# Kernel tuning notes

Hardware: AMD Instinct MI355X
Metric: run time of the kernel (lower is better)

The kernel has to match this reference:

```python
import jax, jax.numpy as jnp
import numpy as np

N_NODES = 100000
N_EDGES = 1600000
IN_FEATS, HID, NUM_CLS = 128, 128, 40


def setup_inputs() -> dict:
    key = jax.random.key(0)
    ks = jax.random.split(key, 5)
    x = jax.random.normal(ks[0], (N_NODES, IN_FEATS), dtype=jnp.float32)
    # xavier-like scale for weights
    W1 = jax.random.normal(ks[1], (IN_FEATS, HID), dtype=jnp.float32) * (1.0 / np.sqrt(IN_FEATS))
    b1 = jnp.zeros((HID,), dtype=jnp.float32)
    W2 = jax.random.normal(ks[2], (HID, NUM_CLS), dtype=jnp.float32) * (1.0 / np.sqrt(HID))
    b2 = jnp.zeros((NUM_CLS,), dtype=jnp.float32)
    src = jax.random.randint(ks[3], (N_EDGES,), 0, N_NODES, dtype=jnp.int32)
    dst = jax.random.randint(ks[4], (N_EDGES,), 0, N_NODES, dtype=jnp.int32)
    return {"x": x, "W1": W1, "b1": b1, "W2": W2, "b2": b2, "src": src, "dst": dst}


def _graph_conv(h, W, b, src, dst, src_norm, dst_norm, n_nodes):
    # DGL GraphConv, norm='both': D_out^{-1/2} A D_in^{-1/2} H W + b
    # (weight-first vs aggregate-first ordering in DGL is mathematically identical)
    hs = h * src_norm[:, None]                      # [N, d] source-side norm
    msg = hs[src]                                   # [E, d] gather
    agg = jax.ops.segment_sum(msg, dst, num_segments=n_nodes)  # [N, d] scatter-add
    agg = agg * dst_norm[:, None]                   # dest-side norm
    return agg @ W + b


def reference(x, W1, b1, W2, b2, src, dst):
    n = x.shape[0]
    ones = jnp.ones(src.shape[0], dtype=x.dtype)
    out_deg = jnp.clip(jax.ops.segment_sum(ones, src, num_segments=n), 1.0)
    in_deg = jnp.clip(jax.ops.segment_sum(ones, dst, num_segments=n), 1.0)
    src_norm = out_deg ** -0.5
    dst_norm = in_deg ** -0.5
    h = jax.nn.relu(_graph_conv(x, W1, b1, src, dst, src_norm, dst_norm, n))
    return _graph_conv(h, W2, b2, src, dst, src_norm, dst_norm, n)
```

## Files before the change

kernel.cpp:

```cpp
#include <hip/hip_runtime.h>

constexpr int NN   = 100000;
constexpr int NE   = 1600000;
constexpr int INF  = 128;
constexpr int NC   = 40;
constexpr int HPAD = 64;

constexpr int BKSH = 9;
constexpr int NBK  = (NN + 511) / 512;
constexpr int CAPB = 10240;
constexpr int EPB  = 4096;
constexpr int PBLK = (NE + EPB - 1) / EPB;
constexpr int CVB  = 6250;
constexpr int ATS  = 136;

typedef __attribute__((ext_vector_type(8))) short short8;
typedef __attribute__((ext_vector_type(4))) float f32x4;

__device__ __forceinline__ float bflo(unsigned int u) { return __uint_as_float(u << 16); }
__device__ __forceinline__ float bfhi(unsigned int u) { return __uint_as_float(u & 0xffff0000u); }
__device__ __forceinline__ unsigned short f2bf(float f) {
    unsigned int u = __float_as_uint(f);
    return (unsigned short)((u + 0x7fffu + ((u >> 16) & 1u)) >> 16);
}
__device__ __forceinline__ unsigned int pack2(float a, float b) {
    return (unsigned int)f2bf(a) | ((unsigned int)f2bf(b) << 16);
}

__global__ __launch_bounds__(256) void partconv_kernel(const int* __restrict__ src,
                                                       const int* __restrict__ dst,
                                                       int* __restrict__ curD_g,
                                                       int* __restrict__ curS_g,
                                                       int* __restrict__ epartsD,
                                                       unsigned short* __restrict__ epartsS,
                                                       const float* __restrict__ x,
                                                       unsigned short* __restrict__ xh,
                                                       const float* __restrict__ W1,
                                                       const float* __restrict__ W2,
                                                       unsigned short* __restrict__ w1t,
                                                       unsigned short* __restrict__ w2t) {
    const int tid = threadIdx.x;
    if (blockIdx.x >= PBLK) {
        int cb = blockIdx.x - PBLK;
        if (cb < CVB) {
            int j = cb * 256 + tid;
            float4 v0 = ((const float4*)x)[2 * j];
            float4 v1 = ((const float4*)x)[2 * j + 1];
            uint4 o;
            o.x = pack2(v0.x, v0.y);
            o.y = pack2(v0.z, v0.w);
            o.z = pack2(v1.x, v1.y);
            o.w = pack2(v1.z, v1.w);
            ((uint4*)xh)[j] = o;
        } else if (cb == CVB) {
            for (int i = tid; i < 128 * 128; i += 256) {
                int k = i >> 7, n = i & 127;
                w1t[n * 128 + k] = f2bf(W1[i]);
            }
        } else {
            for (int i = tid; i < 48 * 128; i += 256) {
                int n = i >> 7, k = i & 127;
                w2t[i] = f2bf((n < NC) ? W2[k * NC + n] : 0.f);
            }
        }
        return;
    }
    __shared__ int sc[256];
    __shared__ int cntD[NBK], gadjD[NBK], curD[NBK];
    __shared__ int cntS[NBK], gadjS[NBK], curS[NBK];
    __shared__ int stageD[EPB];
    __shared__ unsigned short stageS[EPB];
    __shared__ unsigned char bidD[EPB];
    __shared__ unsigned char bidS[EPB];
    const int e0 = blockIdx.x * EPB;
    const int total = min(EPB, NE - e0);

    for (int i = tid; i < NBK; i += 256) { cntD[i] = 0; cntS[i] = 0; }
    __syncthreads();
    for (int i = tid; i < total; i += 256) {
        atomicAdd(&cntD[dst[e0 + i] >> BKSH], 1);
        atomicAdd(&cntS[src[e0 + i] >> BKSH], 1);
    }
    __syncthreads();
    {
        int v = (tid < NBK) ? cntD[tid] : 0;
        sc[tid] = v;
        __syncthreads();
        for (int off = 1; off < 256; off <<= 1) {
            int t = (tid >= off) ? sc[tid - off] : 0;
            __syncthreads();
            sc[tid] += t;
            __syncthreads();
        }
        if (tid < NBK) {
            int excl = sc[tid] - v;
            curD[tid] = excl;
            int g = (v > 0) ? atomicAdd(&curD_g[tid], v) : 0;
            gadjD[tid] = tid * CAPB + g - excl;
        }
        __syncthreads();
        v = (tid < NBK) ? cntS[tid] : 0;
        sc[tid] = v;
        __syncthreads();
        for (int off = 1; off < 256; off <<= 1) {
            int t = (tid >= off) ? sc[tid - off] : 0;
            __syncthreads();
            sc[tid] += t;
            __syncthreads();
        }
        if (tid < NBK) {
            int excl = sc[tid] - v;
            curS[tid] = excl;
            int g = (v > 0) ? atomicAdd(&curS_g[tid], v) : 0;
            gadjS[tid] = tid * CAPB + g - excl;
        }
    }
    __syncthreads();
    for (int i = tid; i < total; i += 256) {
        int s = src[e0 + i];
        int d = dst[e0 + i];
        int bD = d >> BKSH;
        int offD = atomicAdd(&curD[bD], 1);
        stageD[offD] = s | ((d - (bD << BKSH)) << 17);
        bidD[offD] = (unsigned char)bD;
        int bS = s >> BKSH;
        int offS = atomicAdd(&curS[bS], 1);
        stageS[offS] = (unsigned short)(s - (bS << BKSH));
        bidS[offS] = (unsigned char)bS;
    }
    __syncthreads();
    for (int j = tid; j < total; j += 256) {
        int b = bidD[j];
        epartsD[gadjD[b] + j] = stageD[j];
    }
    for (int j = tid; j < total; j += 256) {
        int b = bidS[j];
        epartsS[gadjS[b] + j] = stageS[j];
    }
}

__global__ __launch_bounds__(1024) void pass2_kernel(const int* __restrict__ epartsD,
                                                     const unsigned short* __restrict__ epartsS,
                                                     const int* __restrict__ curD_g,
                                                     const int* __restrict__ curS_g,
                                                     int* __restrict__ row_beg,
                                                     int* __restrict__ row_end,
                                                     int* __restrict__ esrc,
                                                     float* __restrict__ srcn,
                                                     float* __restrict__ dstn) {
    __shared__ int hist[512];
    __shared__ int cur[512];
    __shared__ int histS[512];
    __shared__ int lesrc[CAPB];
    const int tid = threadIdx.x;
    const int b = blockIdx.x;

    const int base  = b * CAPB;
    const int cnt   = curD_g[b];
    const int cntS  = curS_g[b];
    const int n0 = b << BKSH;
    const int nloc = min(512, NN - n0);

    if (tid < 512) { hist[tid] = 0; histS[tid] = 0; }
    __syncthreads();
    for (int j = tid; j < cnt; j += 1024)
        atomicAdd(&hist[epartsD[base + j] >> 17], 1);
    for (int j = tid; j < cntS; j += 1024)
        atomicAdd(&histS[(int)epartsS[base + j]], 1);
    __syncthreads();
    int myc  = (tid < 512) ? hist[tid] : 0;
    int mycS = (tid < 512) ? histS[tid] : 0;
    for (int off = 1; off < 512; off <<= 1) {
        int t = (tid < 512 && tid >= off) ? hist[tid - off] : 0;
        __syncthreads();
        if (tid < 512) hist[tid] += t;
        __syncthreads();
    }
    if (tid < 512) {
        int excl = hist[tid] - myc;
        cur[tid] = excl;
        if (tid < nloc) {
            int g = n0 + tid;
            row_beg[g] = base + excl;
            row_end[g] = base + excl + myc;
            dstn[g] = rsqrtf(fmaxf((float)myc, 1.0f));
            srcn[g] = rsqrtf(fmaxf((float)mycS, 1.0f));
        }
    }
    __syncthreads();
    for (int j = tid; j < cnt; j += 1024) {
        int rec = epartsD[base + j];
        int pos = atomicAdd(&cur[rec >> 17], 1);
        lesrc[pos] = rec & 0x1FFFF;
    }
    __syncthreads();
    for (int j = tid; j < cnt; j += 1024) esrc[base + j] = lesrc[j];
}

__global__ __launch_bounds__(256, 8) void fused_kernel(const int* __restrict__ row_beg,
                                                       const int* __restrict__ row_end,
                                                       const int* __restrict__ esrc,
                                                       const unsigned short* __restrict__ xh,
                                                       const float* __restrict__ srcn,
                                                       const unsigned short* __restrict__ w1t,
                                                       const unsigned short* __restrict__ w2t,
                                                       const float* __restrict__ b1,
                                                       const float* __restrict__ dstn,
                                                       unsigned short* __restrict__ hwb) {
    __shared__ unsigned short At[32 * ATS];
    __shared__ float dn[32], sn[32], b1l[128];
    const int tid  = threadIdx.x;
    const int r0   = blockIdx.x * 32;
    const int wv   = tid >> 6;
    const int lane = tid & 63;

    if (tid < 32) {
        int r = r0 + tid;
        dn[tid] = (r < NN) ? dstn[r] : 0.f;
        sn[tid] = (r < NN) ? srcn[r] : 0.f;
    }
    if (tid >= 64 && tid < 192) b1l[tid - 64] = b1[tid - 64];
    __syncthreads();

    const int quad = lane >> 4;
    const int l16  = lane & 15;
    for (int i = 0; i < 8; ++i) {
        const int node = r0 + wv * 8 + i;
        float a0 = 0.f, a1 = 0.f, a2 = 0.f, a3 = 0.f;
        float a4 = 0.f, a5 = 0.f, a6 = 0.f, a7 = 0.f;
        if (node < NN) {
            int beg = __builtin_amdgcn_readfirstlane(row_beg[node]);
            int end = __builtin_amdgcn_readfirstlane(row_end[node]);
            for (int e = beg; e < end; e += 16) {
                const int rem = end - e;
                int s[4];
#pragma unroll
                for (int t = 0; t < 4; ++t) {
                    int slot = t * 4 + quad;
                    s[t] = esrc[(slot < rem) ? (e + slot) : beg];
                }
                float n[4];
                uint4 u[4];
#pragma unroll
                for (int t = 0; t < 4; ++t) {
                    int slot = t * 4 + quad;
                    n[t] = (slot < rem) ? srcn[s[t]] : 0.f;
                    u[t] = ((const uint4*)(xh + (size_t)s[t] * INF))[l16];
                }
#pragma unroll
                for (int t = 0; t < 4; ++t) {
                    a0 += bflo(u[t].x) * n[t]; a1 += bfhi(u[t].x) * n[t];
                    a2 += bflo(u[t].y) * n[t]; a3 += bfhi(u[t].y) * n[t];
                    a4 += bflo(u[t].z) * n[t]; a5 += bfhi(u[t].z) * n[t];
                    a6 += bflo(u[t].w) * n[t]; a7 += bfhi(u[t].w) * n[t];
                }
            }
        }
        a0 += __shfl_down(a0, 32); a1 += __shfl_down(a1, 32);
        a2 += __shfl_down(a2, 32); a3 += __shfl_down(a3, 32);
        a4 += __shfl_down(a4, 32); a5 += __shfl_down(a5, 32);
        a6 += __shfl_down(a6, 32); a7 += __shfl_down(a7, 32);
        a0 += __shfl_down(a0, 16); a1 += __shfl_down(a1, 16);
        a2 += __shfl_down(a2, 16); a3 += __shfl_down(a3, 16);
        a4 += __shfl_down(a4, 16); a5 += __shfl_down(a5, 16);
        a6 += __shfl_down(a6, 16); a7 += __shfl_down(a7, 16);
        if (lane < 16) {
            uint4 o;
            o.x = pack2(a0, a1);
            o.y = pack2(a2, a3);
            o.z = pack2(a4, a5);
            o.w = pack2(a6, a7);
            *(uint4*)&At[(wv * 8 + i) * ATS + l16 * 8] = o;
        }
    }
    __syncthreads();

    const int lrow  = lane & 15;
    const int lquad = lane >> 4;
    const int rt    = wv >> 1;
    const int ntB   = (wv & 1) * 4;

    short8 afrag[4];
#pragma unroll
    for (int ks = 0; ks < 4; ++ks)
        afrag[ks] = *(const short8*)&At[(rt * 16 + lrow) * ATS + ks * 32 + lquad * 8];
    __syncthreads();

    float hreg[4][4];
#pragma unroll
    for (int nt2 = 0; nt2 < 4; ++nt2) {
        f32x4 acc = {0.f, 0.f, 0.f, 0.f};
#pragma unroll
        for (int ks = 0; ks < 4; ++ks) {
            short8 bfr = *(const short8*)&w1t[((ntB + nt2) * 16 + lrow) * 128 + ks * 32 + lquad * 8];
            acc = __builtin_amdgcn_mfma_f32_16x16x32_bf16(afrag[ks], bfr, acc, 0, 0, 0);
        }
#pragma unroll
        for (int i = 0; i < 4; ++i) hreg[nt2][i] = acc[i];
    }
#pragma unroll
    for (int nt2 = 0; nt2 < 4; ++nt2) {
        int col = (ntB + nt2) * 16 + lrow;
        float bb = b1l[col];
#pragma unroll
        for (int i = 0; i < 4; ++i) {
            int row = rt * 16 + lquad * 4 + i;
            At[row * ATS + col] = f2bf(fmaxf(hreg[nt2][i] * dn[row] + bb, 0.f));
        }
    }
    __syncthreads();

    if ((wv & 1) == 0) {
        short8 hf[4];
#pragma unroll
        for (int ks = 0; ks < 4; ++ks)
            hf[ks] = *(const short8*)&At[(rt * 16 + lrow) * ATS + ks * 32 + lquad * 8];
#pragma unroll
        for (int nt = 0; nt < 3; ++nt) {
            f32x4 acc = {0.f, 0.f, 0.f, 0.f};
#pragma unroll
            for (int ks = 0; ks < 4; ++ks) {
                short8 bfr = *(const short8*)&w2t[(nt * 16 + lrow) * 128 + ks * 32 + lquad * 8];
                acc = __builtin_amdgcn_mfma_f32_16x16x32_bf16(hf[ks], bfr, acc, 0, 0, 0);
            }
            int col = nt * 16 + lrow;
            if (col < NC) {
#pragma unroll
                for (int i = 0; i < 4; ++i) {
                    int row = rt * 16 + lquad * 4 + i;
                    int grow = r0 + row;
                    if (grow < NN)
                        hwb[(size_t)grow * HPAD + col] = f2bf(acc[i] * sn[row]);
                }
            }
        }
    }
}

__global__ __launch_bounds__(256) void gather2_kernel(const int* __restrict__ row_beg,
                                                      const int* __restrict__ row_end,
                                                      const int* __restrict__ esrc,
                                                      const unsigned short* __restrict__ hwb,
                                                      const float* __restrict__ dst_norm,
                                                      const float* __restrict__ b2,
                                                      float* __restrict__ out) {
    int node = (blockIdx.x * blockDim.x + threadIdx.x) >> 6;
    int lane = threadIdx.x & 63;
    if (node >= NN) return;
    int beg = __builtin_amdgcn_readfirstlane(row_beg[node]);
    int end = __builtin_amdgcn_readfirstlane(row_end[node]);
    const int g = lane >> 3;
    const int j = lane & 7;
    float a0 = 0.f, a1 = 0.f, a2 = 0.f, a3 = 0.f;
    float a4 = 0.f, a5 = 0.f, a6 = 0.f, a7 = 0.f;
    for (int e = beg; e < end; e += 32) {
        const int rem = end - e;
        int s[4];
        float m[4];
#pragma unroll
        for (int q = 0; q < 4; ++q) {
            int slot = q * 8 + g;
            bool v = (slot < rem);
            s[q] = esrc[v ? (e + slot) : beg];
            m[q] = v ? 1.f : 0.f;
        }
        uint4 u[4];
#pragma unroll
        for (int q = 0; q < 4; ++q)
            u[q] = ((const uint4*)(hwb + (size_t)s[q] * HPAD))[j];
#pragma unroll
        for (int q = 0; q < 4; ++q) {
            a0 += bflo(u[q].x) * m[q]; a1 += bfhi(u[q].x) * m[q];
            a2 += bflo(u[q].y) * m[q]; a3 += bfhi(u[q].y) * m[q];
            a4 += bflo(u[q].z) * m[q]; a5 += bfhi(u[q].z) * m[q];
            a6 += bflo(u[q].w) * m[q]; a7 += bfhi(u[q].w) * m[q];
        }
    }
    a0 += __shfl_down(a0, 32); a1 += __shfl_down(a1, 32);
    a2 += __shfl_down(a2, 32); a3 += __shfl_down(a3, 32);
    a4 += __shfl_down(a4, 32); a5 += __shfl_down(a5, 32);
    a6 += __shfl_down(a6, 32); a7 += __shfl_down(a7, 32);
    a0 += __shfl_down(a0, 16); a1 += __shfl_down(a1, 16);
    a2 += __shfl_down(a2, 16); a3 += __shfl_down(a3, 16);
    a4 += __shfl_down(a4, 16); a5 += __shfl_down(a5, 16);
    a6 += __shfl_down(a6, 16); a7 += __shfl_down(a7, 16);
    a0 += __shfl_down(a0, 8);  a1 += __shfl_down(a1, 8);
    a2 += __shfl_down(a2, 8);  a3 += __shfl_down(a3, 8);
    a4 += __shfl_down(a4, 8);  a5 += __shfl_down(a5, 8);
    a6 += __shfl_down(a6, 8);  a7 += __shfl_down(a7, 8);
    if (lane < 5) {
        float dnv = dst_norm[node];
        float4 bb0 = ((const float4*)b2)[2 * lane];
        float4 bb1 = ((const float4*)b2)[2 * lane + 1];
        float4 o0, o1;
        o0.x = a0 * dnv + bb0.x;
        o0.y = a1 * dnv + bb0.y;
        o0.z = a2 * dnv + bb0.z;
        o0.w = a3 * dnv + bb0.w;
        o1.x = a4 * dnv + bb1.x;
        o1.y = a5 * dnv + bb1.y;
        o1.z = a6 * dnv + bb1.z;
        o1.w = a7 * dnv + bb1.w;
        float4* op = (float4*)(out + (size_t)node * NC);
        op[2 * lane]     = o0;
        op[2 * lane + 1] = o1;
    }
}

extern "C" void kernel_launch(void* const* d_in, const int* in_sizes, int n_in,
                              void* d_out, int out_size, void* d_ws, size_t ws_size,
                              hipStream_t stream) {
    const float* x   = (const float*)d_in[0];
    const float* W1  = (const float*)d_in[1];
    const float* b1  = (const float*)d_in[2];
    const float* W2  = (const float*)d_in[3];
    const float* b2  = (const float*)d_in[4];
    const int*   src = (const int*)d_in[5];
    const int*   dst = (const int*)d_in[6];
    float* out = (float*)d_out;

    float* srcn = (float*)d_ws;
    int* curDg = (int*)(srcn + NN);
    int* curSg = curDg + 256;
    int* row_beg = curSg + 256;
    int* row_end = row_beg + NN;
    float* dstn  = (float*)(row_end + NN);
    int* esrc    = (int*)(dstn + NN);
    size_t ofs = (size_t)NN + 512 + 3 * (size_t)NN + (size_t)NBK * CAPB;
    ofs = (ofs + 3) & ~(size_t)3;
    unsigned short* xh   = (unsigned short*)((float*)d_ws + ofs);
    unsigned short* w1t  = xh + (size_t)NN * INF;
    unsigned short* w2t  = w1t + 128 * 128;
    unsigned short* hwb  = w2t + 48 * 128;

    int* epartsD = (int*)d_out;
    unsigned short* epartsS = (unsigned short*)(epartsD + (size_t)NBK * CAPB);

    hipMemsetAsync(curDg, 0, 512 * sizeof(int), stream);

    partconv_kernel<<<PBLK + CVB + 2, 256, 0, stream>>>(src, dst, curDg, curSg,
                                                        epartsD, epartsS,
                                                        x, xh, W1, W2, w1t, w2t);
    pass2_kernel<<<NBK, 1024, 0, stream>>>(epartsD, epartsS, curDg, curSg,
                                           row_beg, row_end, esrc, srcn, dstn);
    fused_kernel<<<(NN + 31) / 32, 256, 0, stream>>>(row_beg, row_end, esrc, xh,
                                                     srcn, w1t, w2t, b1, dstn, hwb);
    gather2_kernel<<<(NN * 64 + 255) / 256, 256, 0, stream>>>(row_beg, row_end,
                                                              esrc, hwb,
                                                              dstn, b2, out);
}
```

Before: 272.8 us.

## Move x/weight bf16 conversion into pass2 and speed up partition scan

The x/W1/W2 bf16 conversion blocks move from the partition kernel into the pass2 kernel, so the conversion now overlaps the per-bucket CSR build instead of the edge partitioning. The partition kernel keeps src/dst in registers between the count and scatter passes, which avoids a second global read. It also replaces the two barrier-heavy shared-memory scans with a wavefront shuffle scan that handles both histograms at once. The cost is higher register pressure (32 ints per thread) and 1024-thread conversion blocks sharing the launch with the heavy pass2 blocks.

```diff
diff --git a/kernel.cpp b/kernel.cpp
--- a/kernel.cpp
+++ b/kernel.cpp
@@ -11,7 +11,7 @@
 constexpr int CAPB = 10240;
 constexpr int EPB  = 4096;
 constexpr int PBLK = (NE + EPB - 1) / EPB;
-constexpr int CVB  = 6250;
+constexpr int CVB4 = 1563;
 constexpr int ATS  = 136;
 
 typedef __attribute__((ext_vector_type(8))) short short8;
@@ -27,106 +27,82 @@
     return (unsigned int)f2bf(a) | ((unsigned int)f2bf(b) << 16);
 }
 
-__global__ __launch_bounds__(256) void partconv_kernel(const int* __restrict__ src,
-                                                       const int* __restrict__ dst,
-                                                       int* __restrict__ curD_g,
-                                                       int* __restrict__ curS_g,
-                                                       int* __restrict__ epartsD,
-                                                       unsigned short* __restrict__ epartsS,
-                                                       const float* __restrict__ x,
-                                                       unsigned short* __restrict__ xh,
-                                                       const float* __restrict__ W1,
-                                                       const float* __restrict__ W2,
-                                                       unsigned short* __restrict__ w1t,
-                                                       unsigned short* __restrict__ w2t) {
-    const int tid = threadIdx.x;
-    if (blockIdx.x >= PBLK) {
-        int cb = blockIdx.x - PBLK;
-        if (cb < CVB) {
-            int j = cb * 256 + tid;
-            float4 v0 = ((const float4*)x)[2 * j];
-            float4 v1 = ((const float4*)x)[2 * j + 1];
-            uint4 o;
-            o.x = pack2(v0.x, v0.y);
-            o.y = pack2(v0.z, v0.w);
-            o.z = pack2(v1.x, v1.y);
-            o.w = pack2(v1.z, v1.w);
-            ((uint4*)xh)[j] = o;
-        } else if (cb == CVB) {
-            for (int i = tid; i < 128 * 128; i += 256) {
-                int k = i >> 7, n = i & 127;
-                w1t[n * 128 + k] = f2bf(W1[i]);
-            }
-        } else {
-            for (int i = tid; i < 48 * 128; i += 256) {
-                int n = i >> 7, k = i & 127;
-                w2t[i] = f2bf((n < NC) ? W2[k * NC + n] : 0.f);
-            }
-        }
-        return;
-    }
-    __shared__ int sc[256];
+__global__ __launch_bounds__(256) void part_kernel(const int* __restrict__ src,
+                                                   const int* __restrict__ dst,
+                                                   int* __restrict__ curD_g,
+                                                   int* __restrict__ curS_g,
+                                                   int* __restrict__ epartsD,
+                                                   unsigned short* __restrict__ epartsS) {
     __shared__ int cntD[NBK], gadjD[NBK], curD[NBK];
     __shared__ int cntS[NBK], gadjS[NBK], curS[NBK];
     __shared__ int stageD[EPB];
     __shared__ unsigned short stageS[EPB];
     __shared__ unsigned char bidD[EPB];
     __shared__ unsigned char bidS[EPB];
+    __shared__ int wtot[8];
+    const int tid = threadIdx.x;
     const int e0 = blockIdx.x * EPB;
     const int total = min(EPB, NE - e0);
 
     for (int i = tid; i < NBK; i += 256) { cntD[i] = 0; cntS[i] = 0; }
     __syncthreads();
-    for (int i = tid; i < total; i += 256) {
-        atomicAdd(&cntD[dst[e0 + i] >> BKSH], 1);
-        atomicAdd(&cntS[src[e0 + i] >> BKSH], 1);
+    int se[16], de[16];
+#pragma unroll
+    for (int k = 0; k < 16; ++k) {
+        int i = tid + k * 256;
+        se[k] = 0; de[k] = 0;
+        if (i < total) {
+            int s = src[e0 + i];
+            int d = dst[e0 + i];
+            se[k] = s; de[k] = d;
+            atomicAdd(&cntD[d >> BKSH], 1);
+            atomicAdd(&cntS[s >> BKSH], 1);
+        }
     }
     __syncthreads();
     {
-        int v = (tid < NBK) ? cntD[tid] : 0;
-        sc[tid] = v;
+        const int lane = tid & 63;
+        const int w = tid >> 6;
+        int vD = (tid < NBK) ? cntD[tid] : 0;
+        int vS = (tid < NBK) ? cntS[tid] : 0;
+        int xD = vD, xS = vS;
+#pragma unroll
+        for (int off = 1; off < 64; off <<= 1) {
+            int tD = __shfl_up(xD, off);
+            int tS = __shfl_up(xS, off);
+            if (lane >= off) { xD += tD; xS += tS; }
+        }
+        if (lane == 63) { wtot[w] = xD; wtot[4 + w] = xS; }
         __syncthreads();
-        for (int off = 1; off < 256; off <<= 1) {
-            int t = (tid >= off) ? sc[tid - off] : 0;
-            __syncthreads();
-            sc[tid] += t;
-            __syncthreads();
-        }
+        int pD = 0, pS = 0;
+        for (int i = 0; i < w; ++i) { pD += wtot[i]; pS += wtot[4 + i]; }
         if (tid < NBK) {
-            int excl = sc[tid] - v;
-            curD[tid] = excl;
-            int g = (v > 0) ? atomicAdd(&curD_g[tid], v) : 0;
-            gadjD[tid] = tid * CAPB + g - excl;
-        }
-        __syncthreads();
-        v = (tid < NBK) ? cntS[tid] : 0;
-        sc[tid] = v;
-        __syncthreads();
-        for (int off = 1; off < 256; off <<= 1) {
-            int t = (tid >= off) ? sc[tid - off] : 0;
-            __syncthreads();
-            sc[tid] += t;
-            __syncthreads();
-        }
-        if (tid < NBK) {
-            int excl = sc[tid] - v;
-            curS[tid] = excl;
-            int g = (v > 0) ? atomicAdd(&curS_g[tid], v) : 0;
-            gadjS[tid] = tid * CAPB + g - excl;
-        }
-    }
-    __syncthreads();
-    for (int i = tid; i < total; i += 256) {
-        int s = src[e0 + i];
-        int d = dst[e0 + i];
-        int bD = d >> BKSH;
-        int offD = atomicAdd(&curD[bD], 1);
-        stageD[offD] = s | ((d - (bD << BKSH)) << 17);
-        bidD[offD] = (unsigned char)bD;
-        int bS = s >> BKSH;
-        int offS = atomicAdd(&curS[bS], 1);
-        stageS[offS] = (unsigned short)(s - (bS << BKSH));
-        bidS[offS] = (unsigned char)bS;
+            int exclD = xD + pD - vD;
+            curD[tid] = exclD;
+            int g = (vD > 0) ? atomicAdd(&curD_g[tid], vD) : 0;
+            gadjD[tid] = tid * CAPB + g - exclD;
+            int exclS = xS + pS - vS;
+            curS[tid] = exclS;
+            int g2 = (vS > 0) ? atomicAdd(&curS_g[tid], vS) : 0;
+            gadjS[tid] = tid * CAPB + g2 - exclS;
+        }
+    }
+    __syncthreads();
+#pragma unroll
+    for (int k = 0; k < 16; ++k) {
+        int i = tid + k * 256;
+        if (i < total) {
+            int s = se[k];
+            int d = de[k];
+            int bD = d >> BKSH;
+            int offD = atomicAdd(&curD[bD], 1);
+            stageD[offD] = s | ((d - (bD << BKSH)) << 17);
+            bidD[offD] = (unsigned char)bD;
+            int bS = s >> BKSH;
+            int offS = atomicAdd(&curS[bS], 1);
+            stageS[offS] = (unsigned short)(s - (bS << BKSH));
+            bidS[offS] = (unsigned char)bS;
+        }
     }
     __syncthreads();
     for (int j = tid; j < total; j += 256) {
@@ -139,21 +115,55 @@
     }
 }
 
-__global__ __launch_bounds__(1024) void pass2_kernel(const int* __restrict__ epartsD,
-                                                     const unsigned short* __restrict__ epartsS,
-                                                     const int* __restrict__ curD_g,
-                                                     const int* __restrict__ curS_g,
-                                                     int* __restrict__ row_beg,
-                                                     int* __restrict__ row_end,
-                                                     int* __restrict__ esrc,
-                                                     float* __restrict__ srcn,
-                                                     float* __restrict__ dstn) {
+__global__ __launch_bounds__(1024) void pass2conv_kernel(const int* __restrict__ epartsD,
+                                                         const unsigned short* __restrict__ epartsS,
+                                                         const int* __restrict__ curD_g,
+                                                         const int* __restrict__ curS_g,
+                                                         int* __restrict__ row_beg,
+                                                         int* __restrict__ row_end,
+                                                         int* __restrict__ esrc,
+                                                         float* __restrict__ srcn,
+                                                         float* __restrict__ dstn,
+                                                         const float* __restrict__ x,
+                                                         unsigned short* __restrict__ xh,
+                                                         const float* __restrict__ W1,
+                                                         const float* __restrict__ W2,
+                                                         unsigned short* __restrict__ w1t,
+                                                         unsigned short* __restrict__ w2t) {
+    const int tid = threadIdx.x;
+    const int blk = blockIdx.x;
+    if (blk >= NBK) {
+        int cb = blk - NBK;
+        if (cb < CVB4) {
+            int j = cb * 1024 + tid;
+            if (j < NN * INF / 8) {
+                float4 v0 = ((const float4*)x)[2 * j];
+                float4 v1 = ((const float4*)x)[2 * j + 1];
+                uint4 o;
+                o.x = pack2(v0.x, v0.y);
+                o.y = pack2(v0.z, v0.w);
+                o.z = pack2(v1.x, v1.y);
+                o.w = pack2(v1.z, v1.w);
+                ((uint4*)xh)[j] = o;
+            }
+        } else if (cb == CVB4) {
+            for (int i = tid; i < 128 * 128; i += 1024) {
+                int k = i >> 7, n = i & 127;
+                w1t[n * 128 + k] = f2bf(W1[i]);
+            }
+        } else {
+            for (int i = tid; i < 48 * 128; i += 1024) {
+                int n = i >> 7, k = i & 127;
+                w2t[i] = f2bf((n < NC) ? W2[k * NC + n] : 0.f);
+            }
+        }
+        return;
+    }
     __shared__ int hist[512];
     __shared__ int cur[512];
     __shared__ int histS[512];
     __shared__ int lesrc[CAPB];
-    const int tid = threadIdx.x;
-    const int b = blockIdx.x;
+    const int b = blk;
 
     const int base  = b * CAPB;
     const int cnt   = curD_g[b];
@@ -438,11 +448,13 @@
 
     hipMemsetAsync(curDg, 0, 512 * sizeof(int), stream);
 
-    partconv_kernel<<<PBLK + CVB + 2, 256, 0, stream>>>(src, dst, curDg, curSg,
-                                                        epartsD, epartsS,
-                                                        x, xh, W1, W2, w1t, w2t);
-    pass2_kernel<<<NBK, 1024, 0, stream>>>(epartsD, epartsS, curDg, curSg,
-                                           row_beg, row_end, esrc, srcn, dstn);
+    part_kernel<<<PBLK, 256, 0, stream>>>(src, dst, curDg, curSg,
+                                          epartsD, epartsS);
+    pass2conv_kernel<<<NBK + CVB4 + 2, 1024, 0, stream>>>(epartsD, epartsS,
+                                                          curDg, curSg,
+                                                          row_beg, row_end, esrc,
+                                                          srcn, dstn,
+                                                          x, xh, W1, W2, w1t, w2t);
     fused_kernel<<<(NN + 31) / 32, 256, 0, stream>>>(row_beg, row_end, esrc, xh,
                                                      srcn, w1t, w2t, b1, dstn, hwb);
     gather2_kernel<<<(NN * 64 + 255) / 256, 256, 0, stream>>>(row_beg, row_end,
```

After: 263.2 us. 3.5% less time.
